# Optimization experiments

Measured on AMD Instinct MI355X. Metric: run time of the kernel, lower is better.

## Reference

```python
import jax, jax.numpy as jnp
import numpy as np

B, N = 4096, 128
STATE_DIM, GOAL_DIM, OBSTACLE_DIM = 6, 6, 4
VEH = 2 * STATE_DIM + GOAL_DIM  # 18


def setup_inputs() -> dict:
    key = jax.random.key(0)
    ks = jax.random.split(key, 8)
    s = lambda k, shp, fan: jax.random.normal(k, shp, jnp.float32) / np.sqrt(fan)
    return {
        "obs": jax.random.normal(ks[0], (B, 138), jnp.float32),
        "obstacles": jax.random.uniform(ks[1], (B, 5, N), jnp.float32),
        "act": jax.random.normal(ks[2], (B, 2), jnp.float32),
        "ow1": s(ks[3], (22, 256), 22),
        "ob1": jnp.zeros((256,), jnp.float32),
        "ow2": s(ks[4], (256, 256), 256),
        "ob2": jnp.zeros((256,), jnp.float32),
        "qw1": s(ks[5], (396, 256), 396),
        "qb1": jnp.zeros((256,), jnp.float32),
        "qw2": s(ks[6], (256, 256), 256),
        "qb2": jnp.zeros((256,), jnp.float32),
        "qw3": s(ks[7], (256, 1), 256),
        "qb3": jnp.zeros((1,), jnp.float32),
    }


def reference(obs, obstacles, act, ow1, ob1, ow2, ob2, qw1, qb1, qw2, qb2, qw3, qb3):
    # obs: [B, 138]; obstacles: [B, obstacle_dim+1, N]; act: [B, 2]
    veh = obs[:, :VEH]                                 # [B, 18]
    obst_data = obstacles[:, :OBSTACLE_DIM, :]         # [B, 4, N]
    mask = obstacles[:, -1, :]                         # [B, N]
    # per-obstacle features: concat broadcast vehicle state with obstacle data -> [B, N, 22]
    x = jnp.concatenate(
        [jnp.broadcast_to(veh[:, None, :], (veh.shape[0], obst_data.shape[2], VEH)),
         obst_data.transpose(0, 2, 1)], axis=-1)
    # shared obstacle MLP (ReLU on both layers, incl. output_activation)
    h = jax.nn.relu(jnp.einsum("bnf,fh->bnh", x, ow1) + ob1)
    h = jax.nn.relu(jnp.einsum("bnh,hk->bnk", h, ow2) + ob2)  # [B, N, 256]
    # masked sum-pool over obstacle axis
    pooled = jnp.einsum("bnh,bn->bh", h, mask)         # [B, 256]
    comb = jnp.concatenate([obs, pooled, act], axis=-1)  # [B, 396]
    q = jax.nn.relu(comb @ qw1 + qb1)
    q = jax.nn.relu(q @ qw2 + qb2)
    q = q @ qw3 + qb3                                   # [B, 1]
    return jnp.squeeze(q, -1)
```

## Files before the change

kernel.cpp:

```cpp
#include <hip/hip_runtime.h>
#include <hip/hip_bf16.h>


typedef __attribute__((ext_vector_type(8))) short short8;
typedef __attribute__((ext_vector_type(4))) float f32x4;

#define MFMA16(A, B, C) __builtin_amdgcn_mfma_f32_16x16x32_bf16(A, B, C, 0, 0, 0)

__device__ __forceinline__ unsigned short f2b(float f) {
  __hip_bfloat16 h = __float2bfloat16(f);
  return __builtin_bit_cast(unsigned short, h);
}
__device__ __forceinline__ float b2f(unsigned short u) {
  unsigned v = ((unsigned)u) << 16;
  return __builtin_bit_cast(float, v);
}
__device__ __forceinline__ unsigned pk2f(float a, float b) {
  unsigned ua = __builtin_bit_cast(unsigned, a) + 0x8000u;
  unsigned ub = __builtin_bit_cast(unsigned, b) + 0x8000u;
  return __builtin_amdgcn_perm(ub, ua, 0x07060302u);
}

__global__ __launch_bounds__(256) void pack_weights(
    const float* __restrict__ ow1, const float* __restrict__ ow2,
    const float* __restrict__ qw1, const float* __restrict__ qw2,
    unsigned short* __restrict__ ow1q, unsigned short* __restrict__ ow2p,
    unsigned short* __restrict__ qw1h, unsigned short* __restrict__ qw1l,
    unsigned short* __restrict__ qw2h, unsigned short* __restrict__ qw2l) {
  int i = blockIdx.x * 256 + threadIdx.x;
  if (i < 8192) {
    int j = i & 7;
    int l15 = (i >> 3) & 15;
    int quad = (i >> 7) & 3;
    int mt = (i >> 9) & 15;
    int k = quad * 8 + j;
    float v = (k < 22) ? ow1[k * 256 + (mt * 16 + l15)] : 0.f;
    ow1q[i] = f2b(v);
  }
  if (i < 65536) {
    int j = i & 7;
    int n = (i >> 3) & 255;
    int qq = i >> 11;
    int k = (qq >> 2) * 32 + (qq & 3) * 8 + j;
    ow2p[i] = f2b(ow2[k * 256 + n]);
    float w = qw2[k * 256 + n];
    unsigned short h = f2b(w);
    qw2h[i] = h;
    qw2l[i] = f2b(w - b2f(h));
  }
  if (i < 106496) {
    int j = i & 7;
    int n = (i >> 3) & 255;
    int qq = i >> 11;
    int k = (qq >> 2) * 32 + (qq & 3) * 8 + j;
    float w = (k < 396) ? qw1[k * 256 + n] : 0.f;
    unsigned short h = f2b(w);
    qw1h[i] = h;
    qw1l[i] = f2b(w - b2f(h));
  }
}

#define XSTR 40
#define HSTR 272

__global__ __launch_bounds__(512, 4) void obstacle_kernel(
    const float* __restrict__ obs, const float* __restrict__ obstacles,
    const unsigned short* __restrict__ ow1q,
    const unsigned short* __restrict__ ow2p,
    const float* __restrict__ ob1, const float* __restrict__ ob2,
    unsigned short* __restrict__ poolH, unsigned short* __restrict__ poolL) {
  __shared__ __align__(16) unsigned short xs[128 * XSTR];
  __shared__ __align__(16) unsigned short h1[128 * HSTR];
  __shared__ float maskS[128];
  __shared__ unsigned short vehB[32];

  const int b = blockIdx.x;
  const int tid = threadIdx.x;

  if (tid < 18) vehB[tid] = f2b(obs[b * 138 + tid]);
  if (tid < 128) maskS[tid] = obstacles[b * 640 + 512 + tid];
  __syncthreads();

  if (tid < 256) {
    int n = tid >> 1;
    int half = tid & 1;
    unsigned short* wr = &xs[n * XSTR + half * 16];
    if (half == 0) {
      unsigned short r01[16];
#pragma unroll
      for (int k = 0; k < 16; k++) r01[k] = vehB[k];
      *(short8*)(wr + 0) = *(short8*)&r01[0];
      *(short8*)(wr + 8) = *(short8*)&r01[8];
    } else {
      unsigned short r2[8];
      r2[0] = vehB[16];
      r2[1] = vehB[17];
#pragma unroll
      for (int d = 0; d < 4; d++)
        r2[2 + d] = f2b(obstacles[b * 640 + d * 128 + n]);
      r2[6] = 0; r2[7] = 0;
      *(short8*)(wr + 0) = *(short8*)&r2[0];
      short8 z = {0, 0, 0, 0, 0, 0, 0, 0};
      *(short8*)(wr + 8) = z;
    }
  }
  __syncthreads();

  const int wave = tid >> 6;
  const int lane = tid & 63;
  const int quad = lane >> 4;
  const int l15 = lane & 15;

  {
    const unsigned short* wp = &ow1q[wave * 1024 + quad * 128 + l15 * 8];
    short8 wfr[2];
#pragma unroll
    for (int i = 0; i < 2; i++) wfr[i] = *(const short8*)(wp + i * 512);

    const unsigned short* bxp = &xs[l15 * XSTR + quad * 8];
    short8 bx[8];
#pragma unroll
    for (int nt = 0; nt < 8; nt++)
      bx[nt] = *(const short8*)(bxp + nt * 16 * XSTR);

    unsigned short* wrb = &h1[l15 * HSTR + wave * 32 + quad * 4];

#pragma unroll
    for (int i = 0; i < 2; i++) {
      f32x4 cinit = *(const f32x4*)&ob1[wave * 32 + i * 16 + quad * 4];
      f32x4 acc1[8];
#pragma unroll
      for (int nt = 0; nt < 8; nt++) acc1[nt] = MFMA16(wfr[i], bx[nt], cinit);
#pragma unroll
      for (int nt = 0; nt < 8; nt++) {
        float v0 = fmaxf(acc1[nt][0], 0.f);
        float v1 = fmaxf(acc1[nt][1], 0.f);
        float v2 = fmaxf(acc1[nt][2], 0.f);
        float v3 = fmaxf(acc1[nt][3], 0.f);
        uint2 pk;
        pk.x = pk2f(v0, v1);
        pk.y = pk2f(v2, v3);
        *(uint2*)(wrb + nt * 16 * HSTR + i * 16) = pk;
      }
    }
  }
  __syncthreads();

  f32x4 acc[8][2];
#pragma unroll
  for (int t = 0; t < 2; t++) {
    float bv = ob2[wave * 32 + t * 16 + l15];
    f32x4 bvec = {bv, bv, bv, bv};
#pragma unroll
    for (int mt = 0; mt < 8; mt++) acc[mt][t] = bvec;
  }

  const unsigned short* bp = &ow2p[(quad * 256 + wave * 32 + l15) * 8];
  const unsigned short* h1r = &h1[l15 * HSTR + quad * 8];
  short8 bcur[2], bnxt[2];
#pragma unroll
  for (int t = 0; t < 2; t++) bcur[t] = *(const short8*)(bp + t * 128);

#pragma unroll 1
  for (int kb = 0; kb < 8; kb++) {
    if (kb < 7) {
#pragma unroll
      for (int t = 0; t < 2; t++)
        bnxt[t] = *(const short8*)(bp + 8192 + t * 128);
    }
    short8 afr[8];
#pragma unroll
    for (int mt = 0; mt < 8; mt++)
      afr[mt] = *(const short8*)(h1r + mt * 16 * HSTR);
#pragma unroll
    for (int mt = 0; mt < 8; mt++)
#pragma unroll
      for (int t = 0; t < 2; t++) acc[mt][t] = MFMA16(afr[mt], bcur[t], acc[mt][t]);
    bp += 8192;
    h1r += 32;
    if (kb < 7) {
#pragma unroll
      for (int t = 0; t < 2; t++) bcur[t] = bnxt[t];
    }
  }

  f32x4 mk[8];
  const float* mkp = &maskS[quad * 4];
#pragma unroll
  for (int mt = 0; mt < 8; mt++) mk[mt] = *(const f32x4*)(mkp + mt * 16);

#pragma unroll
  for (int t = 0; t < 2; t++) {
    float s = 0.f;
#pragma unroll
    for (int mt = 0; mt < 8; mt++) {
#pragma unroll
      for (int r = 0; r < 4; r++) {
        float v = fmaxf(acc[mt][t][r], 0.f);
        s = fmaf(mk[mt][r], v, s);
      }
    }
    s += __shfl_xor(s, 16);
    s += __shfl_xor(s, 32);
    if (quad == 0) {
      int n = wave * 32 + t * 16 + l15;
      unsigned short sh = (unsigned short)(__builtin_bit_cast(unsigned, s) >> 16);
      poolH[b * 256 + n] = sh;
      poolL[b * 256 + n] = f2b(s - b2f(sh));
    }
  }
}

__global__ __launch_bounds__(1024) void head_mfma(
    const float* __restrict__ obs, const float* __restrict__ act,
    const unsigned short* __restrict__ poolH,
    const unsigned short* __restrict__ poolL,
    const unsigned short* __restrict__ qw1h,
    const unsigned short* __restrict__ qw1l,
    const unsigned short* __restrict__ qw2h,
    const unsigned short* __restrict__ qw2l,
    const float* __restrict__ qb1, const float* __restrict__ qb2,
    const float* __restrict__ qw3, const float* __restrict__ qb3,
    float* __restrict__ out) {
  const int CSTR = 424;
  const int HSTRQ = 272;
  __shared__ unsigned short combH[16 * 424], combL[16 * 424];
  __shared__ unsigned short h1H[16 * 272], h1L[16 * 272];
  __shared__ float wred[16][16];

  const int tid = threadIdx.x;
  const int r0 = blockIdx.x * 16;
  const int wave = tid >> 6;
  const int lane = tid & 63;
  const int quad = lane >> 4;
  const int l15 = lane & 15;
  const int n = wave * 16 + l15;

  const unsigned short* w1h = &qw1h[(quad * 256 + n) * 8];
  const unsigned short* w1l = &qw1l[(quad * 256 + n) * 8];
  const unsigned short* w2h = &qw2h[(quad * 256 + n) * 8];
  const unsigned short* w2l = &qw2l[(quad * 256 + n) * 8];

  short8 bh[2], bl[2];
  bh[0] = *(const short8*)(w1h);
  bl[0] = *(const short8*)(w1l);
  bh[1] = *(const short8*)(w1h + 8192);
  bl[1] = *(const short8*)(w1l + 8192);

  for (int idx = tid; idx < 16 * 416; idx += 1024) {
    int m = idx / 416;
    int k = idx - m * 416;
    unsigned short hi, lo;
    if (k < 138) {
      float v = obs[(r0 + m) * 138 + k];
      hi = f2b(v);
      lo = f2b(v - b2f(hi));
    } else if (k < 394) {
      hi = poolH[(r0 + m) * 256 + (k - 138)];
      lo = poolL[(r0 + m) * 256 + (k - 138)];
    } else if (k < 396) {
      float v = act[(r0 + m) * 2 + (k - 394)];
      hi = f2b(v);
      lo = f2b(v - b2f(hi));
    } else {
      hi = 0; lo = 0;
    }
    combH[m * CSTR + k] = hi;
    combL[m * CSTR + k] = lo;
  }
  __syncthreads();

  f32x4 acc = {0.f, 0.f, 0.f, 0.f}, accm = {0.f, 0.f, 0.f, 0.f};
#pragma unroll
  for (int kb = 0; kb < 13; kb++) {
    const int c = kb & 1;
    short8 ch = bh[c];
    short8 cl = bl[c];
    if (kb + 2 < 13) {
      bh[c] = *(const short8*)(w1h + (kb + 2) * 8192);
      bl[c] = *(const short8*)(w1l + (kb + 2) * 8192);
    }
    int ao = l15 * CSTR + kb * 32 + quad * 8;
    short8 ah = *(const short8*)&combH[ao];
    short8 al = *(const short8*)&combL[ao];
    acc = MFMA16(ah, ch, acc);
    accm = MFMA16(ah, cl, accm);
    accm = MFMA16(al, ch, accm);
  }
  {
    float bias = qb1[n];
#pragma unroll
    for (int r = 0; r < 4; r++) {
      int m = quad * 4 + r;
      float v = fmaxf(acc[r] + accm[r] + bias, 0.f);
      unsigned short hi = f2b(v);
      h1H[m * HSTRQ + n] = hi;
      h1L[m * HSTRQ + n] = f2b(v - b2f(hi));
    }
  }

  short8 dh[2], dl[2];
  dh[0] = *(const short8*)(w2h);
  dl[0] = *(const short8*)(w2l);
  dh[1] = *(const short8*)(w2h + 8192);
  dl[1] = *(const short8*)(w2l + 8192);

  __syncthreads();

  f32x4 a2 = {0.f, 0.f, 0.f, 0.f}, a2m = {0.f, 0.f, 0.f, 0.f};
#pragma unroll
  for (int kb = 0; kb < 8; kb++) {
    const int c = kb & 1;
    short8 ch = dh[c];
    short8 cl = dl[c];
    if (kb + 2 < 8) {
      dh[c] = *(const short8*)(w2h + (kb + 2) * 8192);
      dl[c] = *(const short8*)(w2l + (kb + 2) * 8192);
    }
    int ao = l15 * HSTRQ + kb * 32 + quad * 8;
    short8 ah = *(const short8*)&h1H[ao];
    short8 al = *(const short8*)&h1L[ao];
    a2 = MFMA16(ah, ch, a2);
    a2m = MFMA16(ah, cl, a2m);
    a2m = MFMA16(al, ch, a2m);
  }

  {
    float w3 = qw3[n];
    float qb2n = qb2[n];
#pragma unroll
    for (int r = 0; r < 4; r++) {
      float v = fmaxf(a2[r] + a2m[r] + qb2n, 0.f);
      float s = v * w3;
      s += __shfl_xor(s, 1);
      s += __shfl_xor(s, 2);
      s += __shfl_xor(s, 4);
      s += __shfl_xor(s, 8);
      if (l15 == 0) wred[wave][quad * 4 + r] = s;
    }
  }
  __syncthreads();
  if (tid < 16) {
    float s = qb3[0];
#pragma unroll
    for (int w = 0; w < 16; w++) s += wred[w][tid];
    out[r0 + tid] = s;
  }
}

extern "C" void kernel_launch(void* const* d_in, const int* in_sizes, int n_in,
                              void* d_out, int out_size, void* d_ws, size_t ws_size,
                              hipStream_t stream) {
  const float* obs       = (const float*)d_in[0];
  const float* obstacles = (const float*)d_in[1];
  const float* act       = (const float*)d_in[2];
  const float* ow1       = (const float*)d_in[3];
  const float* ob1       = (const float*)d_in[4];
  const float* ow2       = (const float*)d_in[5];
  const float* ob2       = (const float*)d_in[6];
  const float* qw1       = (const float*)d_in[7];
  const float* qb1       = (const float*)d_in[8];
  const float* qw2       = (const float*)d_in[9];
  const float* qb2       = (const float*)d_in[10];
  const float* qw3       = (const float*)d_in[11];
  const float* qb3       = (const float*)d_in[12];
  float* out = (float*)d_out;

  unsigned short* ow1q = (unsigned short*)d_ws;
  unsigned short* ow2p = ow1q + 8192;
  unsigned short* qw1h = ow2p + 65536;
  unsigned short* qw1l = qw1h + 106496;
  unsigned short* qw2h = qw1l + 106496;
  unsigned short* qw2l = qw2h + 65536;
  unsigned short* poolH = qw2l + 65536;
  unsigned short* poolL = poolH + 1048576;

  pack_weights<<<416, 256, 0, stream>>>(ow1, ow2, qw1, qw2, ow1q, ow2p, qw1h,
                                        qw1l, qw2h, qw2l);
  obstacle_kernel<<<4096, 512, 0, stream>>>(obs, obstacles, ow1q, ow2p, ob1,
                                            ob2, poolH, poolL);
  head_mfma<<<256, 1024, 0, stream>>>(obs, act, poolH, poolL, qw1h, qw1l,
                                      qw2h, qw2l, qb1, qb2, qw3, qb3, out);
}
```

Baseline: 166.4 us.

## Split obstacle pooling across two half-obstacle blocks with fp32 partial sums

The obstacle kernel now runs two 256-thread blocks per batch row instead of one 512-thread block. Each block handles 64 obstacles, and each wave covers 64 output channels with a 4x4 MFMA tile in place of 8x2. Each block writes an fp32 partial pooled vector, and the head kernel adds the two partials before its hi/lo bf16 split. This gives smaller blocks with less LDS each, which should raise occupancy and improve per-wave B-fragment reuse, at the cost of a second reduction pass and extra pool traffic.

Result: slower. 176.1 us (+5.8%).

```diff
diff --git a/kernel.cpp b/kernel.cpp
--- a/kernel.cpp
+++ b/kernel.cpp
@@ -63,29 +63,31 @@
 #define XSTR 40
 #define HSTR 272
 
-__global__ __launch_bounds__(512, 4) void obstacle_kernel(
+__global__ __launch_bounds__(256, 4) void obstacle_kernel(
     const float* __restrict__ obs, const float* __restrict__ obstacles,
     const unsigned short* __restrict__ ow1q,
     const unsigned short* __restrict__ ow2p,
     const float* __restrict__ ob1, const float* __restrict__ ob2,
-    unsigned short* __restrict__ poolH, unsigned short* __restrict__ poolL) {
-  __shared__ __align__(16) unsigned short xs[128 * XSTR];
-  __shared__ __align__(16) unsigned short h1[128 * HSTR];
-  __shared__ float maskS[128];
+    float* __restrict__ poolF) {
+  __shared__ __align__(16) unsigned short xs[64 * XSTR];
+  __shared__ __align__(16) unsigned short h1[64 * HSTR];
+  __shared__ float maskS[64];
   __shared__ unsigned short vehB[32];
 
-  const int b = blockIdx.x;
+  const int bb = blockIdx.x;
+  const int b = bb >> 1;
+  const int half = bb & 1;
   const int tid = threadIdx.x;
 
   if (tid < 18) vehB[tid] = f2b(obs[b * 138 + tid]);
-  if (tid < 128) maskS[tid] = obstacles[b * 640 + 512 + tid];
-  __syncthreads();
-
-  if (tid < 256) {
+  if (tid < 64) maskS[tid] = obstacles[b * 640 + 512 + half * 64 + tid];
+  __syncthreads();
+
+  if (tid < 128) {
     int n = tid >> 1;
-    int half = tid & 1;
-    unsigned short* wr = &xs[n * XSTR + half * 16];
-    if (half == 0) {
+    int hf = tid & 1;
+    unsigned short* wr = &xs[n * XSTR + hf * 16];
+    if (hf == 0) {
       unsigned short r01[16];
 #pragma unroll
       for (int k = 0; k < 16; k++) r01[k] = vehB[k];
@@ -97,7 +99,7 @@
       r2[1] = vehB[17];
 #pragma unroll
       for (int d = 0; d < 4; d++)
-        r2[2 + d] = f2b(obstacles[b * 640 + d * 128 + n]);
+        r2[2 + d] = f2b(obstacles[b * 640 + d * 128 + half * 64 + n]);
       r2[6] = 0; r2[7] = 0;
       *(short8*)(wr + 0) = *(short8*)&r2[0];
       short8 z = {0, 0, 0, 0, 0, 0, 0, 0};
@@ -112,88 +114,88 @@
   const int l15 = lane & 15;
 
   {
-    const unsigned short* wp = &ow1q[wave * 1024 + quad * 128 + l15 * 8];
-    short8 wfr[2];
-#pragma unroll
-    for (int i = 0; i < 2; i++) wfr[i] = *(const short8*)(wp + i * 512);
+    const unsigned short* wp = &ow1q[wave * 2048 + quad * 128 + l15 * 8];
+    short8 wfr[4];
+#pragma unroll
+    for (int g = 0; g < 4; g++) wfr[g] = *(const short8*)(wp + g * 512);
 
     const unsigned short* bxp = &xs[l15 * XSTR + quad * 8];
-    short8 bx[8];
-#pragma unroll
-    for (int nt = 0; nt < 8; nt++)
-      bx[nt] = *(const short8*)(bxp + nt * 16 * XSTR);
-
-    unsigned short* wrb = &h1[l15 * HSTR + wave * 32 + quad * 4];
-
-#pragma unroll
-    for (int i = 0; i < 2; i++) {
-      f32x4 cinit = *(const f32x4*)&ob1[wave * 32 + i * 16 + quad * 4];
-      f32x4 acc1[8];
-#pragma unroll
-      for (int nt = 0; nt < 8; nt++) acc1[nt] = MFMA16(wfr[i], bx[nt], cinit);
-#pragma unroll
-      for (int nt = 0; nt < 8; nt++) {
-        float v0 = fmaxf(acc1[nt][0], 0.f);
-        float v1 = fmaxf(acc1[nt][1], 0.f);
-        float v2 = fmaxf(acc1[nt][2], 0.f);
-        float v3 = fmaxf(acc1[nt][3], 0.f);
+    short8 bx[4];
+#pragma unroll
+    for (int mt = 0; mt < 4; mt++)
+      bx[mt] = *(const short8*)(bxp + mt * 16 * XSTR);
+
+    unsigned short* wrb = &h1[l15 * HSTR + wave * 64 + quad * 4];
+
+#pragma unroll
+    for (int g = 0; g < 4; g++) {
+      f32x4 cinit = *(const f32x4*)&ob1[wave * 64 + g * 16 + quad * 4];
+      f32x4 acc1[4];
+#pragma unroll
+      for (int mt = 0; mt < 4; mt++) acc1[mt] = MFMA16(wfr[g], bx[mt], cinit);
+#pragma unroll
+      for (int mt = 0; mt < 4; mt++) {
+        float v0 = fmaxf(acc1[mt][0], 0.f);
+        float v1 = fmaxf(acc1[mt][1], 0.f);
+        float v2 = fmaxf(acc1[mt][2], 0.f);
+        float v3 = fmaxf(acc1[mt][3], 0.f);
         uint2 pk;
         pk.x = pk2f(v0, v1);
         pk.y = pk2f(v2, v3);
-        *(uint2*)(wrb + nt * 16 * HSTR + i * 16) = pk;
+        *(uint2*)(wrb + mt * 16 * HSTR + g * 16) = pk;
       }
     }
   }
   __syncthreads();
 
-  f32x4 acc[8][2];
-#pragma unroll
-  for (int t = 0; t < 2; t++) {
-    float bv = ob2[wave * 32 + t * 16 + l15];
+  f32x4 acc[4][4];
+#pragma unroll
+  for (int t = 0; t < 4; t++) {
+    float bv = ob2[wave * 64 + t * 16 + l15];
     f32x4 bvec = {bv, bv, bv, bv};
 #pragma unroll
-    for (int mt = 0; mt < 8; mt++) acc[mt][t] = bvec;
-  }
-
-  const unsigned short* bp = &ow2p[(quad * 256 + wave * 32 + l15) * 8];
+    for (int mt = 0; mt < 4; mt++) acc[mt][t] = bvec;
+  }
+
+  const unsigned short* bp = &ow2p[(quad * 256 + wave * 64 + l15) * 8];
   const unsigned short* h1r = &h1[l15 * HSTR + quad * 8];
-  short8 bcur[2], bnxt[2];
-#pragma unroll
-  for (int t = 0; t < 2; t++) bcur[t] = *(const short8*)(bp + t * 128);
+  short8 bcur[4], bnxt[4];
+#pragma unroll
+  for (int t = 0; t < 4; t++) bcur[t] = *(const short8*)(bp + t * 128);
 
 #pragma unroll 1
   for (int kb = 0; kb < 8; kb++) {
     if (kb < 7) {
 #pragma unroll
-      for (int t = 0; t < 2; t++)
+      for (int t = 0; t < 4; t++)
         bnxt[t] = *(const short8*)(bp + 8192 + t * 128);
     }
-    short8 afr[8];
-#pragma unroll
-    for (int mt = 0; mt < 8; mt++)
+    short8 afr[4];
+#pragma unroll
+    for (int mt = 0; mt < 4; mt++)
       afr[mt] = *(const short8*)(h1r + mt * 16 * HSTR);
 #pragma unroll
-    for (int mt = 0; mt < 8; mt++)
-#pragma unroll
-      for (int t = 0; t < 2; t++) acc[mt][t] = MFMA16(afr[mt], bcur[t], acc[mt][t]);
+    for (int mt = 0; mt < 4; mt++)
+#pragma unroll
+      for (int t = 0; t < 4; t++) acc[mt][t] = MFMA16(afr[mt], bcur[t], acc[mt][t]);
     bp += 8192;
     h1r += 32;
     if (kb < 7) {
 #pragma unroll
-      for (int t = 0; t < 2; t++) bcur[t] = bnxt[t];
-    }
-  }
-
-  f32x4 mk[8];
+      for (int t = 0; t < 4; t++) bcur[t] = bnxt[t];
+    }
+  }
+
+  f32x4 mk[4];
   const float* mkp = &maskS[quad * 4];
 #pragma unroll
-  for (int mt = 0; mt < 8; mt++) mk[mt] = *(const f32x4*)(mkp + mt * 16);
-
-#pragma unroll
-  for (int t = 0; t < 2; t++) {
+  for (int mt = 0; mt < 4; mt++) mk[mt] = *(const f32x4*)(mkp + mt * 16);
+
+#pragma unroll
+  for (int t = 0; t < 4; t++) {
     float s = 0.f;
 #pragma unroll
-    for (int mt = 0; mt < 8; mt++) {
+    for (int mt = 0; mt < 4; mt++) {
 #pragma unroll
       for (int r = 0; r < 4; r++) {
         float v = fmaxf(acc[mt][t][r], 0.f);
@@ -203,18 +205,15 @@
     s += __shfl_xor(s, 16);
     s += __shfl_xor(s, 32);
     if (quad == 0) {
-      int n = wave * 32 + t * 16 + l15;
-      unsigned short sh = (unsigned short)(__builtin_bit_cast(unsigned, s) >> 16);
-      poolH[b * 256 + n] = sh;
-      poolL[b * 256 + n] = f2b(s - b2f(sh));
+      int n = wave * 64 + t * 16 + l15;
+      poolF[b * 512 + half * 256 + n] = s;
     }
   }
 }
 
 __global__ __launch_bounds__(1024) void head_mfma(
     const float* __restrict__ obs, const float* __restrict__ act,
-    const unsigned short* __restrict__ poolH,
-    const unsigned short* __restrict__ poolL,
+    const float* __restrict__ poolF,
     const unsigned short* __restrict__ qw1h,
     const unsigned short* __restrict__ qw1l,
     const unsigned short* __restrict__ qw2h,
@@ -256,8 +255,10 @@
       hi = f2b(v);
       lo = f2b(v - b2f(hi));
     } else if (k < 394) {
-      hi = poolH[(r0 + m) * 256 + (k - 138)];
-      lo = poolL[(r0 + m) * 256 + (k - 138)];
+      float v = poolF[(r0 + m) * 512 + (k - 138)] +
+                poolF[(r0 + m) * 512 + 256 + (k - 138)];
+      hi = f2b(v);
+      lo = f2b(v - b2f(hi));
     } else if (k < 396) {
       float v = act[(r0 + m) * 2 + (k - 394)];
       hi = f2b(v);
@@ -372,13 +373,12 @@
   unsigned short* qw1l = qw1h + 106496;
   unsigned short* qw2h = qw1l + 106496;
   unsigned short* qw2l = qw2h + 65536;
-  unsigned short* poolH = qw2l + 65536;
-  unsigned short* poolL = poolH + 1048576;
+  float* poolF = (float*)(qw2l + 65536);
 
   pack_weights<<<416, 256, 0, stream>>>(ow1, ow2, qw1, qw2, ow1q, ow2p, qw1h,
                                         qw1l, qw2h, qw2l);
-  obstacle_kernel<<<4096, 512, 0, stream>>>(obs, obstacles, ow1q, ow2p, ob1,
-                                            ob2, poolH, poolL);
-  head_mfma<<<256, 1024, 0, stream>>>(obs, act, poolH, poolL, qw1h, qw1l,
+  obstacle_kernel<<<8192, 256, 0, stream>>>(obs, obstacles, ow1q, ow2p, ob1,
+                                            ob2, poolF);
+  head_mfma<<<256, 1024, 0, stream>>>(obs, act, poolF, qw1h, qw1l,
                                       qw2h, qw2l, qb1, qb2, qw3, qb3, out);
 }
```
